# Performance work log

Measured on AMD Instinct MI355X. Metric: run time of the kernel, lower is better.

## Reference

```python
import jax, jax.numpy as jnp
import numpy as np

D_MODEL = 1024
D_STATE = 16
D_CONV = 4
EXPAND = 2
D_INNER = D_MODEL * EXPAND
B = 2
L = 1024


def setup_inputs() -> dict:
    key = jax.random.key(0)
    ks = jax.random.split(key, 8)
    s = lambda k, shape, scale: jax.random.normal(k, shape, dtype=jnp.float32) * scale
    x = s(ks[0], (B, L, D_MODEL), 1.0)
    W_in = s(ks[1], (2 * D_INNER, D_MODEL), D_MODEL ** -0.5)
    conv_w = s(ks[2], (D_INNER, D_CONV), D_CONV ** -0.5)
    conv_b = s(ks[3], (D_INNER,), 0.02)
    W_x = s(ks[4], (2 * D_STATE + 1, D_INNER), D_INNER ** -0.5)
    dt_w = s(ks[5], (D_INNER, 1), 1.0)
    dt_b = s(ks[6], (D_INNER,), 0.02)
    A_log = jnp.log(jnp.broadcast_to(jnp.arange(1, D_STATE + 1, dtype=jnp.float32), (D_INNER, D_STATE)))
    D_param = jnp.ones((D_INNER,), dtype=jnp.float32)
    W_out = s(ks[7], (D_MODEL, D_INNER), D_INNER ** -0.5)
    return dict(x=x, W_in=W_in, conv_w=conv_w, conv_b=conv_b, W_x=W_x,
                dt_w=dt_w, dt_b=dt_b, A_log=A_log, D_param=D_param, W_out=W_out)


def _causal_dwconv(x, w, b):
    # x: (B,L,D), w: (D,K), b: (D,). torch Conv1d(pad=K-1)[..., :L] == left-pad causal conv.
    K = w.shape[1]
    Lx = x.shape[1]
    xp = jnp.pad(x, ((0, 0), (K - 1, 0), (0, 0)))
    return sum(xp[:, k:k + Lx, :] * w[:, k] for k in range(K)) + b


def reference(x, W_in, conv_w, conv_b, W_x, dt_w, dt_b, A_log, D_param, W_out):
    Bb, Ll, _ = x.shape
    xz = jnp.einsum('bld,ed->ble', x, W_in)          # (B,L,2*D_INNER)
    x_ssm, z = jnp.split(xz, 2, axis=-1)
    xc = jax.nn.silu(_causal_dwconv(x_ssm, conv_w, conv_b))  # (B,L,D_INNER)

    proj = jnp.einsum('bld,ed->ble', xc, W_x)        # (B,L,1+2N)
    dt_raw = proj[..., :1]
    B_vals = proj[..., 1:1 + D_STATE]                # (B,L,N)
    C_vals = proj[..., 1 + D_STATE:]                 # (B,L,N)
    dt = jax.nn.softplus(dt_raw * dt_w[:, 0] + dt_b)  # (B,L,D_INNER)

    A = -jnp.exp(A_log)                              # (D_INNER,N)
    dA = jnp.exp(dt[..., None] * A)                  # (B,L,D,N)
    dBx = dt[..., None] * B_vals[:, :, None, :] * xc[..., None]  # (B,L,D,N)

    def step(h, inputs):
        dA_t, dBx_t, C_t = inputs
        h = dA_t * h + dBx_t                         # (B,D,N)
        y_t = jnp.einsum('bdn,bn->bd', h, C_t)
        return h, y_t

    h0 = jnp.zeros((Bb, D_INNER, D_STATE), dtype=x.dtype)
    xs = (jnp.moveaxis(dA, 1, 0), jnp.moveaxis(dBx, 1, 0), jnp.moveaxis(C_vals, 1, 0))
    _, ys = jax.lax.scan(step, h0, xs)               # ys: (L,B,D)
    y = jnp.moveaxis(ys, 0, 1) + xc * D_param        # skip connection
    y = y * jax.nn.silu(z)
    return jnp.einsum('bld,ed->ble', y, W_out)
```

## Files before the change

kernel.cpp:

```cpp
#include <hip/hip_runtime.h>
#include <cstdint>
#include <cstddef>

#define DM 1024
#define DI 2048
#define DS 16
#define LSEQ 1024
#define NROWS 2048
#define CHUNKS 32
#define CLEN 32
#define PSTRIDE 36
#define NPAD 48
#define KSPLIT 16

typedef __attribute__((ext_vector_type(8))) short short8;
typedef __attribute__((ext_vector_type(4))) float float4v;

__device__ __forceinline__ float bf2f(ushort u) {
  union { float f; uint32_t i; } v; v.i = ((uint32_t)u) << 16; return v.f;
}
__device__ __forceinline__ ushort f2bf(float f) {
  union { float f; uint32_t i; } v; v.f = f;
  uint32_t x = v.i;
  uint32_t r = (x + 0x7fffu + ((x >> 16) & 1u)) >> 16;
  return (ushort)r;
}

__device__ __forceinline__ void gl2lds16(const ushort* g, ushort* l) {
  __builtin_amdgcn_global_load_lds(
      (const __attribute__((address_space(1))) unsigned int*)g,
      (__attribute__((address_space(3))) unsigned int*)l,
      16, 0, 0);
}

#define NX   (NROWS * DM)
#define NWIN (2 * DI * DM)
#define NWOUT (DM * DI)
#define NWX  (33 * DI)
#define NWXP (NPAD * DI)

__global__ __launch_bounds__(256)
void cast_all(const float* __restrict__ x, const float* __restrict__ W_in,
              const float* __restrict__ W_out, const float* __restrict__ Wx,
              ushort* __restrict__ xb, ushort* __restrict__ wib,
              ushort* __restrict__ wob, ushort* __restrict__ wxb) {
  int i = (blockIdx.x * 256 + threadIdx.x) * 8;
  const float* src;
  ushort* dst;
  int off;
  if (i < NX) { src = x; dst = xb; off = 0; }
  else if (i < NX + NWIN) { src = W_in; dst = wib; off = NX; }
  else if (i < NX + NWIN + NWOUT) { src = W_out; dst = wob; off = NX + NWIN; }
  else if (i < NX + NWIN + NWOUT + NWXP) {
    int j = i - (NX + NWIN + NWOUT);
    short8 o;
    if (j < NWX) {
      float4v a = *(const float4v*)(Wx + j);
      float4v b = *(const float4v*)(Wx + j + 4);
#pragma unroll
      for (int k = 0; k < 4; ++k) o[k] = (short)f2bf(a[k]);
#pragma unroll
      for (int k = 0; k < 4; ++k) o[4 + k] = (short)f2bf(b[k]);
    } else {
#pragma unroll
      for (int k = 0; k < 8; ++k) o[k] = 0;
    }
    *(short8*)(wxb + j) = o;
    return;
  } else return;
  int j = i - off;
  float4v a = *(const float4v*)(src + j);
  float4v b = *(const float4v*)(src + j + 4);
  short8 o;
#pragma unroll
  for (int k = 0; k < 4; ++k) o[k] = (short)f2bf(a[k]);
#pragma unroll
  for (int k = 0; k < 4; ++k) o[4 + k] = (short)f2bf(b[k]);
  *(short8*)(dst + j) = o;
}

template <typename OUT_T>
__global__ __launch_bounds__(256, 2)
void gemm_bt(const ushort* __restrict__ A, const ushort* __restrict__ B,
             OUT_T* __restrict__ C, int M, int N, int K, int lda, int ldb) {
  __shared__ ushort As[128 * 64];
  __shared__ ushort Bs[128 * 64];
  const int tid = threadIdx.x;
  const int wave = tid >> 6;
  const int lane = tid & 63;
  const int m16 = lane & 15;
  const int quad = lane >> 4;
  const int row0 = blockIdx.x * 128;
  const int col0 = blockIdx.y * 128;
  const int wm = (wave >> 1) * 64;
  const int wn = (wave & 1) * 64;

  const ushort *Ap[4], *Bp[4];
  ushort *Asd[4], *Bsd[4];
#pragma unroll
  for (int q = 0; q < 4; ++q) {
    int c = tid + 256 * q;
    Ap[q] = A + (size_t)(row0 + (c >> 3)) * lda + (c & 7) * 8;
    Bp[q] = B + (size_t)(col0 + (c >> 3)) * ldb + (c & 7) * 8;
    Asd[q] = As + c * 8;
    Bsd[q] = Bs + c * 8;
  }

  float4v acc[4][4] = {};

  for (int k0 = 0; k0 < K; k0 += 64) {
    __syncthreads();
#pragma unroll
    for (int q = 0; q < 4; ++q) gl2lds16(Ap[q], Asd[q]);
#pragma unroll
    for (int q = 0; q < 4; ++q) gl2lds16(Bp[q], Bsd[q]);
#pragma unroll
    for (int q = 0; q < 4; ++q) { Ap[q] += 64; Bp[q] += 64; }
    __syncthreads();

#pragma unroll
    for (int kk = 0; kk < 64; kk += 32) {
      short8 af[4], bfr[4];
#pragma unroll
      for (int i = 0; i < 4; ++i)
        af[i] = *(const short8*)&As[(wm + i * 16 + m16) * 64 + kk + quad * 8];
#pragma unroll
      for (int j = 0; j < 4; ++j)
        bfr[j] = *(const short8*)&Bs[(wn + j * 16 + m16) * 64 + kk + quad * 8];
#pragma unroll
      for (int i = 0; i < 4; ++i)
#pragma unroll
        for (int j = 0; j < 4; ++j)
          acc[i][j] = __builtin_amdgcn_mfma_f32_16x16x32_bf16(af[i], bfr[j], acc[i][j], 0, 0, 0);
    }
  }

#pragma unroll
  for (int i = 0; i < 4; ++i) {
#pragma unroll
    for (int r = 0; r < 4; ++r) {
      int row = row0 + wm + i * 16 + quad * 4 + r;
#pragma unroll
      for (int j = 0; j < 4; ++j) {
        int col = col0 + wn + j * 16 + m16;
        float v = acc[i][j][r];
        if constexpr (sizeof(OUT_T) == 4)
          C[(size_t)row * N + col] = v;
        else
          C[(size_t)row * N + col] = f2bf(v);
      }
    }
  }
}

__global__ __launch_bounds__(256, 2)
void gemm_bt64(const ushort* __restrict__ A, const ushort* __restrict__ B,
               float* __restrict__ C, int M, int N, int K, int lda, int ldb) {
  __shared__ ushort As[64 * 32];
  __shared__ ushort Bs[64 * 32];
  const int tid = threadIdx.x;
  const int wave = tid >> 6;
  const int lane = tid & 63;
  const int m16 = lane & 15;
  const int quad = lane >> 4;
  const int row0 = blockIdx.x * 64;
  const int col0 = blockIdx.y * 64;
  const int wm = (wave >> 1) * 32;
  const int wn = (wave & 1) * 32;

  const int c = tid;
  const ushort* Ap = A + (size_t)(row0 + (c >> 2)) * lda + (c & 3) * 8;
  const ushort* Bp = B + (size_t)(col0 + (c >> 2)) * ldb + (c & 3) * 8;
  ushort* Asd = As + c * 8;
  ushort* Bsd = Bs + c * 8;

  float4v acc[2][2] = {};

  for (int k0 = 0; k0 < K; k0 += 32) {
    __syncthreads();
    gl2lds16(Ap, Asd);
    gl2lds16(Bp, Bsd);
    Ap += 32; Bp += 32;
    __syncthreads();

    short8 af[2], bfr[2];
#pragma unroll
    for (int i = 0; i < 2; ++i)
      af[i] = *(const short8*)&As[(wm + i * 16 + m16) * 32 + quad * 8];
#pragma unroll
    for (int j = 0; j < 2; ++j)
      bfr[j] = *(const short8*)&Bs[(wn + j * 16 + m16) * 32 + quad * 8];
#pragma unroll
    for (int i = 0; i < 2; ++i)
#pragma unroll
      for (int j = 0; j < 2; ++j)
        acc[i][j] = __builtin_amdgcn_mfma_f32_16x16x32_bf16(af[i], bfr[j], acc[i][j], 0, 0, 0);
  }

#pragma unroll
  for (int i = 0; i < 2; ++i) {
#pragma unroll
    for (int r = 0; r < 4; ++r) {
      int row = row0 + wm + i * 16 + quad * 4 + r;
#pragma unroll
      for (int j = 0; j < 2; ++j) {
        int col = col0 + wn + j * 16 + m16;
        C[(size_t)row * N + col] = acc[i][j][r];
      }
    }
  }
}

__global__ __launch_bounds__(256)
void conv_silu_kernel(const ushort* __restrict__ xz,
                      const float* __restrict__ conv_w,
                      const float* __restrict__ conv_b,
                      ushort* __restrict__ xc) {
  int idx = blockIdx.x * 256 + threadIdx.x;
  int row = idx >> 8;
  int d8 = (idx & 255) << 3;
  int l = row & (LSEQ - 1);
  float acc[8];
  float w[8][4];
#pragma unroll
  for (int j = 0; j < 8; ++j) {
    acc[j] = conv_b[d8 + j];
    float4v wv = *(const float4v*)(conv_w + (d8 + j) * 4);
#pragma unroll
    for (int k = 0; k < 4; ++k) w[j][k] = wv[k];
  }
#pragma unroll
  for (int k = 0; k < 4; ++k) {
    int ls = l - 3 + k;
    if (ls >= 0) {
      short8 xr = *(const short8*)(xz + (size_t)(row - 3 + k) * (2 * DI) + d8);
#pragma unroll
      for (int j = 0; j < 8; ++j) acc[j] += bf2f((ushort)xr[j]) * w[j][k];
    }
  }
  short8 o;
#pragma unroll
  for (int j = 0; j < 8; ++j) {
    float v = acc[j];
    v = v / (1.f + __expf(-v));
    o[j] = (short)f2bf(v);
  }
  *(short8*)(xc + (size_t)row * DI + d8) = o;
}

__global__ __launch_bounds__(256, 2)
void proj_mfma(const ushort* __restrict__ A, const ushort* __restrict__ B,
               float* __restrict__ part) {
  __shared__ ushort As[128 * 32];
  __shared__ ushort Bs[NPAD * 32];
  const int tid = threadIdx.x;
  const int wave = tid >> 6;
  const int lane = tid & 63;
  const int m16 = lane & 15;
  const int quad = lane >> 4;
  const int row0 = blockIdx.x * 128;
  const int koff = blockIdx.z * (DI / KSPLIT);
  const int wm = wave * 32;

  const int c0 = tid, c1 = tid + 256;
  const ushort* Ap0 = A + (size_t)(row0 + (c0 >> 2)) * DI + koff + (c0 & 3) * 8;
  const ushort* Ap1 = A + (size_t)(row0 + (c1 >> 2)) * DI + koff + (c1 & 3) * 8;
  const ushort* Bp0 = B + (size_t)(c0 >> 2) * DI + koff + (c0 & 3) * 8;
  ushort* Asd0 = As + c0 * 8;
  ushort* Asd1 = As + c1 * 8;
  ushort* Bsd0 = Bs + c0 * 8;
  const bool doB = tid < 192;

  float4v acc[2][3] = {};

#pragma unroll
  for (int it = 0; it < 4; ++it) {
    __syncthreads();
    gl2lds16(Ap0, Asd0);
    gl2lds16(Ap1, Asd1);
    if (doB) gl2lds16(Bp0, Bsd0);
    Ap0 += 32; Ap1 += 32; Bp0 += 32;
    __syncthreads();

    short8 af[2], bfr[3];
#pragma unroll
    for (int i = 0; i < 2; ++i)
      af[i] = *(const short8*)&As[(wm + i * 16 + m16) * 32 + quad * 8];
#pragma unroll
    for (int j = 0; j < 3; ++j)
      bfr[j] = *(const short8*)&Bs[(j * 16 + m16) * 32 + quad * 8];
#pragma unroll
    for (int i = 0; i < 2; ++i)
#pragma unroll
      for (int j = 0; j < 3; ++j)
        acc[i][j] = __builtin_amdgcn_mfma_f32_16x16x32_bf16(af[i], bfr[j], acc[i][j], 0, 0, 0);
  }

  float* Cp = part + (size_t)blockIdx.z * NROWS * NPAD;
#pragma unroll
  for (int i = 0; i < 2; ++i) {
#pragma unroll
    for (int r = 0; r < 4; ++r) {
      int row = row0 + wm + i * 16 + quad * 4 + r;
#pragma unroll
      for (int j = 0; j < 3; ++j) {
        int col = j * 16 + m16;
        Cp[(size_t)row * NPAD + col] = acc[i][j][r];
      }
    }
  }
}

__global__ __launch_bounds__(256)
void proj_reduce(const float* __restrict__ part, float* __restrict__ proj) {
  int g = blockIdx.x * 256 + threadIdx.x;
  if (g >= NROWS * 33) return;
  int row = g / 33, col = g - row * 33;
  float s = 0.f;
#pragma unroll
  for (int z = 0; z < KSPLIT; ++z)
    s += part[((size_t)z * NROWS + row) * NPAD + col];
  int pc = (col == 0) ? 0 : 3 + col;
  proj[(size_t)row * PSTRIDE + pc] = s;
}


__global__ __launch_bounds__(256)
void scan_pass1(const float* __restrict__ proj,
                const ushort* __restrict__ xc,
                const float* __restrict__ A_log,
                const float* __restrict__ dt_w,
                const float* __restrict__ dt_b,
                float* __restrict__ aprod,
                float* __restrict__ hend) {
  const int d = blockIdx.x * 256 + threadIdx.x;
  const int ch = blockIdx.y;
  const int b = blockIdx.z;
  float A2[16];
#pragma unroll
  for (int i = 0; i < 4; ++i) {
    float4v a = *(const float4v*)(A_log + (size_t)d * DS + i * 4);
#pragma unroll
    for (int j = 0; j < 4; ++j) A2[i * 4 + j] = -__expf(a[j]) * 1.44269504f;
  }
  const float dtw = dt_w[d], dtb = dt_b[d];
  float h[16];
#pragma unroll
  for (int n = 0; n < 16; ++n) h[n] = 0.f;
  float S = 0.f;
  const size_t rowbase = (size_t)b * LSEQ + ch * CLEN;
#pragma unroll 4
  for (int r = 0; r < CLEN; ++r) {
    const float* pr = proj + (rowbase + r) * PSTRIDE;
    float dtraw = pr[0];
    float4v Bv[4];
#pragma unroll
    for (int i = 0; i < 4; ++i) Bv[i] = *(const float4v*)(pr + 4 + 4 * i);
    float xv = bf2f(xc[(rowbase + r) * DI + d]);
    float draw = dtraw * dtw + dtb;
    float dt = (draw > 20.f) ? draw : __logf(1.f + __expf(draw));
    S += dt;
    float dtx = dt * xv;
#pragma unroll
    for (int n = 0; n < 16; ++n) {
      float dA = exp2f(dt * A2[n]);
      h[n] = dA * h[n] + dtx * Bv[n >> 2][n & 3];
    }
  }
  size_t o = ((size_t)(b * CHUNKS + ch) * DS) * DI + d;
#pragma unroll
  for (int n = 0; n < 16; ++n) {
    aprod[o + (size_t)n * DI] = exp2f(A2[n] * S);
    hend[o + (size_t)n * DI] = h[n];
  }
}

__global__ __launch_bounds__(256)
void scan_pass2(float* __restrict__ aprod, const float* __restrict__ hend) {
  int g = blockIdx.x * 256 + threadIdx.x;
  int d = g & (DI - 1);
  int n = (g >> 11) & 15;
  int b = g >> 15;
  float h = 0.f;
  for (int ch = 0; ch < CHUNKS; ++ch) {
    size_t o = ((size_t)((b * CHUNKS + ch) * DS + n)) * DI + d;
    float a = aprod[o];
    float e = hend[o];
    aprod[o] = h;
    h = a * h + e;
  }
}

__global__ __launch_bounds__(256)
void scan_pass3(const float* __restrict__ proj,
                const ushort* __restrict__ xc,
                const ushort* __restrict__ xz,
                const float* __restrict__ A_log,
                const float* __restrict__ dt_w,
                const float* __restrict__ dt_b,
                const float* __restrict__ D_param,
                const float* __restrict__ hstart,
                ushort* __restrict__ y) {
  const int d = blockIdx.x * 256 + threadIdx.x;
  const int ch = blockIdx.y;
  const int b = blockIdx.z;
  float A2[16];
#pragma unroll
  for (int i = 0; i < 4; ++i) {
    float4v a = *(const float4v*)(A_log + (size_t)d * DS + i * 4);
#pragma unroll
    for (int j = 0; j < 4; ++j) A2[i * 4 + j] = -__expf(a[j]) * 1.44269504f;
  }
  const float dtw = dt_w[d], dtb = dt_b[d];
  const float Dp = D_param[d];
  float h[16];
  size_t o = ((size_t)(b * CHUNKS + ch) * DS) * DI + d;
#pragma unroll
  for (int n = 0; n < 16; ++n) h[n] = hstart[o + (size_t)n * DI];
  const size_t rowbase = (size_t)b * LSEQ + ch * CLEN;
#pragma unroll 4
  for (int r = 0; r < CLEN; ++r) {
    const float* pr = proj + (rowbase + r) * PSTRIDE;
    float dtraw = pr[0];
    float4v Bv[4], Cv[4];
#pragma unroll
    for (int i = 0; i < 4; ++i) Bv[i] = *(const float4v*)(pr + 4 + 4 * i);
#pragma unroll
    for (int i = 0; i < 4; ++i) Cv[i] = *(const float4v*)(pr + 20 + 4 * i);
    float xv = bf2f(xc[(rowbase + r) * DI + d]);
    float zv = bf2f(xz[(rowbase + r) * (2 * DI) + DI + d]);
    float draw = dtraw * dtw + dtb;
    float dt = (draw > 20.f) ? draw : __logf(1.f + __expf(draw));
    float dtx = dt * xv;
    float yv = 0.f;
#pragma unroll
    for (int n = 0; n < 16; ++n) {
      float dA = exp2f(dt * A2[n]);
      h[n] = dA * h[n] + dtx * Bv[n >> 2][n & 3];
      yv += h[n] * Cv[n >> 2][n & 3];
    }
    yv += xv * Dp;
    float sz = zv / (1.f + __expf(-zv));
    y[(rowbase + r) * DI + d] = f2bf(yv * sz);
  }
}

extern "C" void kernel_launch(void* const* d_in, const int* in_sizes, int n_in,
                              void* d_out, int out_size, void* d_ws, size_t ws_size,
                              hipStream_t stream) {
  const float* x       = (const float*)d_in[0];
  const float* W_in    = (const float*)d_in[1];
  const float* conv_w  = (const float*)d_in[2];
  const float* conv_b  = (const float*)d_in[3];
  const float* W_x     = (const float*)d_in[4];
  const float* dt_w    = (const float*)d_in[5];
  const float* dt_b    = (const float*)d_in[6];
  const float* A_log   = (const float*)d_in[7];
  const float* D_param = (const float*)d_in[8];
  const float* W_out   = (const float*)d_in[9];
  float* out = (float*)d_out;

  const size_t MB = 1024 * 1024;
  char* ws = (char*)d_ws;
  ushort* xz    = (ushort*)ws;
  ushort* xc    = (ushort*)(ws + 16 * MB);
  float*  proj  = (float*)(ws + 24 * MB);
  ushort* y     = (ushort*)(ws + 25 * MB);
  ushort* xb    = (ushort*)(ws + 33 * MB);
  ushort* wib   = (ushort*)(ws + 37 * MB);
  float*  aprod = (float*)(ws + 33 * MB);
  float*  hend  = (float*)(ws + 41 * MB);
  ushort* wob   = (ushort*)(ws + 49 * MB);
  ushort* wxb   = (ushort*)(ws + 53 * MB);
  float*  ppart = (float*)(ws + 54 * MB);

  dim3 blk(256);
  cast_all<<<dim3(4144), blk, 0, stream>>>(x, W_in, W_out, W_x, xb, wib, wob, wxb);
  gemm_bt<ushort><<<dim3(16, 32), blk, 0, stream>>>(xb, wib, xz, NROWS, 2 * DI, DM, DM, DM);
  conv_silu_kernel<<<dim3(2048), blk, 0, stream>>>(xz, conv_w, conv_b, xc);
  proj_mfma<<<dim3(16, 1, KSPLIT), blk, 0, stream>>>(xc, wxb, ppart);
  proj_reduce<<<dim3((NROWS * 33 + 255) / 256), blk, 0, stream>>>(ppart, proj);
  scan_pass1<<<dim3(8, CHUNKS, 2), blk, 0, stream>>>(proj, xc, A_log, dt_w, dt_b, aprod, hend);
  scan_pass2<<<dim3(256), blk, 0, stream>>>(aprod, hend);
  scan_pass3<<<dim3(8, CHUNKS, 2), blk, 0, stream>>>(proj, xc, xz, A_log, dt_w, dt_b, D_param, aprod, y);
  gemm_bt64<<<dim3(32, 16), blk, 0, stream>>>(y, wob, out, NROWS, DM, DI, DI, DI);
}
```

Before: 235.0 us.

## Fuse conv+SiLU into x_proj GEMM, deepen out-proj K tile, batch scan_pass2 loads

Merges the depthwise causal conv and SiLU into the x_proj MFMA kernel. Each block computes a 128x128 tile of xc, writes it to global memory and LDS, then multiplies it against the matching W_x slice, which removes one launch and a re-read of xc. The output-projection GEMM now stages a K tile of 64 instead of 32, halving the number of barrier-separated load phases. scan_pass2 preloads all 32 chunk values into registers and writes to a separate hstart buffer instead of in place. The cost is more LDS in the fused kernel, which may lower occupancy, and extra register pressure.

```diff
diff --git a/kernel.cpp b/kernel.cpp
--- a/kernel.cpp
+++ b/kernel.cpp
@@ -156,8 +156,8 @@
 __global__ __launch_bounds__(256, 2)
 void gemm_bt64(const ushort* __restrict__ A, const ushort* __restrict__ B,
                float* __restrict__ C, int M, int N, int K, int lda, int ldb) {
-  __shared__ ushort As[64 * 32];
-  __shared__ ushort Bs[64 * 32];
+  __shared__ ushort As[64 * 64];
+  __shared__ ushort Bs[64 * 64];
   const int tid = threadIdx.x;
   const int wave = tid >> 6;
   const int lane = tid & 63;
@@ -168,33 +168,44 @@
   const int wm = (wave >> 1) * 32;
   const int wn = (wave & 1) * 32;
 
-  const int c = tid;
-  const ushort* Ap = A + (size_t)(row0 + (c >> 2)) * lda + (c & 3) * 8;
-  const ushort* Bp = B + (size_t)(col0 + (c >> 2)) * ldb + (c & 3) * 8;
-  ushort* Asd = As + c * 8;
-  ushort* Bsd = Bs + c * 8;
+  const ushort *Ap[2], *Bp[2];
+  ushort *Asd[2], *Bsd[2];
+#pragma unroll
+  for (int q = 0; q < 2; ++q) {
+    int c = tid + 256 * q;
+    Ap[q] = A + (size_t)(row0 + (c >> 3)) * lda + (c & 7) * 8;
+    Bp[q] = B + (size_t)(col0 + (c >> 3)) * ldb + (c & 7) * 8;
+    Asd[q] = As + c * 8;
+    Bsd[q] = Bs + c * 8;
+  }
 
   float4v acc[2][2] = {};
 
-  for (int k0 = 0; k0 < K; k0 += 32) {
+  for (int k0 = 0; k0 < K; k0 += 64) {
     __syncthreads();
-    gl2lds16(Ap, Asd);
-    gl2lds16(Bp, Bsd);
-    Ap += 32; Bp += 32;
+#pragma unroll
+    for (int q = 0; q < 2; ++q) gl2lds16(Ap[q], Asd[q]);
+#pragma unroll
+    for (int q = 0; q < 2; ++q) gl2lds16(Bp[q], Bsd[q]);
+#pragma unroll
+    for (int q = 0; q < 2; ++q) { Ap[q] += 64; Bp[q] += 64; }
     __syncthreads();
 
-    short8 af[2], bfr[2];
-#pragma unroll
-    for (int i = 0; i < 2; ++i)
-      af[i] = *(const short8*)&As[(wm + i * 16 + m16) * 32 + quad * 8];
-#pragma unroll
-    for (int j = 0; j < 2; ++j)
-      bfr[j] = *(const short8*)&Bs[(wn + j * 16 + m16) * 32 + quad * 8];
-#pragma unroll
-    for (int i = 0; i < 2; ++i)
+#pragma unroll
+    for (int kk = 0; kk < 64; kk += 32) {
+      short8 af[2], bfr[2];
+#pragma unroll
+      for (int i = 0; i < 2; ++i)
+        af[i] = *(const short8*)&As[(wm + i * 16 + m16) * 64 + kk + quad * 8];
 #pragma unroll
       for (int j = 0; j < 2; ++j)
-        acc[i][j] = __builtin_amdgcn_mfma_f32_16x16x32_bf16(af[i], bfr[j], acc[i][j], 0, 0, 0);
+        bfr[j] = *(const short8*)&Bs[(wn + j * 16 + m16) * 64 + kk + quad * 8];
+#pragma unroll
+      for (int i = 0; i < 2; ++i)
+#pragma unroll
+        for (int j = 0; j < 2; ++j)
+          acc[i][j] = __builtin_amdgcn_mfma_f32_16x16x32_bf16(af[i], bfr[j], acc[i][j], 0, 0, 0);
+    }
   }
 
 #pragma unroll
@@ -211,84 +222,89 @@
   }
 }
 
-__global__ __launch_bounds__(256)
-void conv_silu_kernel(const ushort* __restrict__ xz,
-                      const float* __restrict__ conv_w,
-                      const float* __restrict__ conv_b,
-                      ushort* __restrict__ xc) {
-  int idx = blockIdx.x * 256 + threadIdx.x;
-  int row = idx >> 8;
-  int d8 = (idx & 255) << 3;
-  int l = row & (LSEQ - 1);
-  float acc[8];
-  float w[8][4];
-#pragma unroll
-  for (int j = 0; j < 8; ++j) {
-    acc[j] = conv_b[d8 + j];
-    float4v wv = *(const float4v*)(conv_w + (d8 + j) * 4);
-#pragma unroll
-    for (int k = 0; k < 4; ++k) w[j][k] = wv[k];
-  }
-#pragma unroll
-  for (int k = 0; k < 4; ++k) {
-    int ls = l - 3 + k;
-    if (ls >= 0) {
-      short8 xr = *(const short8*)(xz + (size_t)(row - 3 + k) * (2 * DI) + d8);
-#pragma unroll
-      for (int j = 0; j < 8; ++j) acc[j] += bf2f((ushort)xr[j]) * w[j][k];
-    }
-  }
-  short8 o;
-#pragma unroll
-  for (int j = 0; j < 8; ++j) {
-    float v = acc[j];
-    v = v / (1.f + __expf(-v));
-    o[j] = (short)f2bf(v);
-  }
-  *(short8*)(xc + (size_t)row * DI + d8) = o;
-}
-
 __global__ __launch_bounds__(256, 2)
-void proj_mfma(const ushort* __restrict__ A, const ushort* __restrict__ B,
-               float* __restrict__ part) {
-  __shared__ ushort As[128 * 32];
-  __shared__ ushort Bs[NPAD * 32];
+void conv_proj_mfma(const ushort* __restrict__ xz,
+                    const float* __restrict__ conv_w,
+                    const float* __restrict__ conv_b,
+                    const ushort* __restrict__ Wx,
+                    ushort* __restrict__ xc,
+                    float* __restrict__ part) {
+  __shared__ ushort As[128 * 128];
+  __shared__ ushort Bs[NPAD * 128];
   const int tid = threadIdx.x;
   const int wave = tid >> 6;
   const int lane = tid & 63;
   const int m16 = lane & 15;
   const int quad = lane >> 4;
   const int row0 = blockIdx.x * 128;
-  const int koff = blockIdx.z * (DI / KSPLIT);
+  const int d0 = blockIdx.z * 128;
+
+  const int dl = (tid & 15) * 8;
+  const int rl = (tid >> 4) * 8;
+  const int d = d0 + dl;
+  const int R = row0 + rl;
+  const bool edge = ((row0 & (LSEQ - 1)) == 0) && (rl == 0);
+
+  float w[8][4], bias[8];
+#pragma unroll
+  for (int j = 0; j < 8; ++j) {
+    bias[j] = conv_b[d + j];
+    float4v wv = *(const float4v*)(conv_w + (size_t)(d + j) * 4);
+#pragma unroll
+    for (int k = 0; k < 4; ++k) w[j][k] = wv[k];
+  }
+
+  float win[3][8];
+#pragma unroll
+  for (int i = 0; i < 3; ++i) {
+    if (edge) {
+#pragma unroll
+      for (int j = 0; j < 8; ++j) win[i][j] = 0.f;
+    } else {
+      short8 v = *(const short8*)(xz + (size_t)(R - 3 + i) * (2 * DI) + d);
+#pragma unroll
+      for (int j = 0; j < 8; ++j) win[i][j] = bf2f((ushort)v[j]);
+    }
+  }
+#pragma unroll
+  for (int r = 0; r < 8; ++r) {
+    short8 cv = *(const short8*)(xz + (size_t)(R + r) * (2 * DI) + d);
+    float cur[8];
+#pragma unroll
+    for (int j = 0; j < 8; ++j) cur[j] = bf2f((ushort)cv[j]);
+    short8 o;
+#pragma unroll
+    for (int j = 0; j < 8; ++j) {
+      float v = bias[j] + win[0][j] * w[j][0] + win[1][j] * w[j][1] +
+                win[2][j] * w[j][2] + cur[j] * w[j][3];
+      v = v / (1.f + __expf(-v));
+      o[j] = (short)f2bf(v);
+    }
+    *(short8*)(xc + (size_t)(R + r) * DI + d) = o;
+    *(short8*)&As[(rl + r) * 128 + dl] = o;
+#pragma unroll
+    for (int j = 0; j < 8; ++j) { win[0][j] = win[1][j]; win[1][j] = win[2][j]; win[2][j] = cur[j]; }
+  }
+
+#pragma unroll
+  for (int q = 0; q < 3; ++q) {
+    int c = tid + 256 * q;
+    gl2lds16(Wx + (size_t)(c >> 4) * DI + d0 + (c & 15) * 8, Bs + c * 8);
+  }
+
+  __syncthreads();
+
   const int wm = wave * 32;
-
-  const int c0 = tid, c1 = tid + 256;
-  const ushort* Ap0 = A + (size_t)(row0 + (c0 >> 2)) * DI + koff + (c0 & 3) * 8;
-  const ushort* Ap1 = A + (size_t)(row0 + (c1 >> 2)) * DI + koff + (c1 & 3) * 8;
-  const ushort* Bp0 = B + (size_t)(c0 >> 2) * DI + koff + (c0 & 3) * 8;
-  ushort* Asd0 = As + c0 * 8;
-  ushort* Asd1 = As + c1 * 8;
-  ushort* Bsd0 = Bs + c0 * 8;
-  const bool doB = tid < 192;
-
   float4v acc[2][3] = {};
-
-#pragma unroll
-  for (int it = 0; it < 4; ++it) {
-    __syncthreads();
-    gl2lds16(Ap0, Asd0);
-    gl2lds16(Ap1, Asd1);
-    if (doB) gl2lds16(Bp0, Bsd0);
-    Ap0 += 32; Ap1 += 32; Bp0 += 32;
-    __syncthreads();
-
+#pragma unroll
+  for (int k0 = 0; k0 < 128; k0 += 32) {
     short8 af[2], bfr[3];
 #pragma unroll
     for (int i = 0; i < 2; ++i)
-      af[i] = *(const short8*)&As[(wm + i * 16 + m16) * 32 + quad * 8];
+      af[i] = *(const short8*)&As[(wm + i * 16 + m16) * 128 + k0 + quad * 8];
 #pragma unroll
     for (int j = 0; j < 3; ++j)
-      bfr[j] = *(const short8*)&Bs[(j * 16 + m16) * 32 + quad * 8];
+      bfr[j] = *(const short8*)&Bs[(j * 16 + m16) * 128 + k0 + quad * 8];
 #pragma unroll
     for (int i = 0; i < 2; ++i)
 #pragma unroll
@@ -303,10 +319,8 @@
     for (int r = 0; r < 4; ++r) {
       int row = row0 + wm + i * 16 + quad * 4 + r;
 #pragma unroll
-      for (int j = 0; j < 3; ++j) {
-        int col = j * 16 + m16;
-        Cp[(size_t)row * NPAD + col] = acc[i][j][r];
-      }
+      for (int j = 0; j < 3; ++j)
+        Cp[(size_t)row * NPAD + j * 16 + m16] = acc[i][j][r];
     }
   }
 }
@@ -376,18 +390,25 @@
 }
 
 __global__ __launch_bounds__(256)
-void scan_pass2(float* __restrict__ aprod, const float* __restrict__ hend) {
+void scan_pass2(const float* __restrict__ aprod, const float* __restrict__ hend,
+                float* __restrict__ hstart) {
   int g = blockIdx.x * 256 + threadIdx.x;
-  int d = g & (DI - 1);
-  int n = (g >> 11) & 15;
-  int b = g >> 15;
+  int dd = g & (DI - 1);
+  int nn = (g >> 11) & 15;
+  int bb = g >> 15;
+  float av[CHUNKS], ev[CHUNKS];
+#pragma unroll
+  for (int c = 0; c < CHUNKS; ++c) {
+    size_t o = ((size_t)((bb * CHUNKS + c) * DS + nn)) * DI + dd;
+    av[c] = aprod[o];
+    ev[c] = hend[o];
+  }
   float h = 0.f;
-  for (int ch = 0; ch < CHUNKS; ++ch) {
-    size_t o = ((size_t)((b * CHUNKS + ch) * DS + n)) * DI + d;
-    float a = aprod[o];
-    float e = hend[o];
-    aprod[o] = h;
-    h = a * h + e;
+#pragma unroll
+  for (int c = 0; c < CHUNKS; ++c) {
+    size_t o = ((size_t)((bb * CHUNKS + c) * DS + nn)) * DI + dd;
+    hstart[o] = h;
+    h = av[c] * h + ev[c];
   }
 }
 
@@ -462,26 +483,26 @@
 
   const size_t MB = 1024 * 1024;
   char* ws = (char*)d_ws;
-  ushort* xz    = (ushort*)ws;
-  ushort* xc    = (ushort*)(ws + 16 * MB);
-  float*  proj  = (float*)(ws + 24 * MB);
-  ushort* y     = (ushort*)(ws + 25 * MB);
-  ushort* xb    = (ushort*)(ws + 33 * MB);
-  ushort* wib   = (ushort*)(ws + 37 * MB);
-  float*  aprod = (float*)(ws + 33 * MB);
-  float*  hend  = (float*)(ws + 41 * MB);
-  ushort* wob   = (ushort*)(ws + 49 * MB);
-  ushort* wxb   = (ushort*)(ws + 53 * MB);
-  float*  ppart = (float*)(ws + 54 * MB);
+  ushort* xz     = (ushort*)ws;
+  ushort* xc     = (ushort*)(ws + 16 * MB);
+  float*  proj   = (float*)(ws + 24 * MB);
+  ushort* y      = (ushort*)(ws + 25 * MB);
+  ushort* xb     = (ushort*)(ws + 33 * MB);
+  ushort* wib    = (ushort*)(ws + 37 * MB);
+  float*  aprod  = (float*)(ws + 45 * MB);
+  float*  hend   = (float*)(ws + 53 * MB);
+  float*  hstart = (float*)(ws + 61 * MB);
+  ushort* wob    = (ushort*)(ws + 69 * MB);
+  ushort* wxb    = (ushort*)(ws + 73 * MB);
+  float*  ppart  = (float*)(ws + 74 * MB);
 
   dim3 blk(256);
   cast_all<<<dim3(4144), blk, 0, stream>>>(x, W_in, W_out, W_x, xb, wib, wob, wxb);
   gemm_bt<ushort><<<dim3(16, 32), blk, 0, stream>>>(xb, wib, xz, NROWS, 2 * DI, DM, DM, DM);
-  conv_silu_kernel<<<dim3(2048), blk, 0, stream>>>(xz, conv_w, conv_b, xc);
-  proj_mfma<<<dim3(16, 1, KSPLIT), blk, 0, stream>>>(xc, wxb, ppart);
+  conv_proj_mfma<<<dim3(16, 1, KSPLIT), blk, 0, stream>>>(xz, conv_w, conv_b, wxb, xc, ppart);
   proj_reduce<<<dim3((NROWS * 33 + 255) / 256), blk, 0, stream>>>(ppart, proj);
   scan_pass1<<<dim3(8, CHUNKS, 2), blk, 0, stream>>>(proj, xc, A_log, dt_w, dt_b, aprod, hend);
-  scan_pass2<<<dim3(256), blk, 0, stream>>>(aprod, hend);
-  scan_pass3<<<dim3(8, CHUNKS, 2), blk, 0, stream>>>(proj, xc, xz, A_log, dt_w, dt_b, D_param, aprod, y);
+  scan_pass2<<<dim3(256), blk, 0, stream>>>(aprod, hend, hstart);
+  scan_pass3<<<dim3(8, CHUNKS, 2), blk, 0, stream>>>(proj, xc, xz, A_log, dt_w, dt_b, D_param, hstart, y);
   gemm_bt64<<<dim3(32, 16), blk, 0, stream>>>(y, wob, out, NROWS, DM, DI, DI, DI);
 }
```

Result: faster. 227.7 us (-3.1%).
